# Performance work log

Measured on AMD Instinct MI355X. Metric: run time of the kernel, lower is better.

The kernel has to match this reference:

```python
import jax, jax.numpy as jnp
import numpy as np

B, T, D = 2, 2048, 1024
H = 16
HD = D // H

def setup_inputs() -> dict:
    key = jax.random.key(0)
    ks = jax.random.split(key, 6)
    s = 1.0 / np.sqrt(D)
    x  = jax.random.normal(ks[0], (B, T, D), dtype=jnp.float32)
    Wq = jax.random.uniform(ks[1], (D, D), jnp.float32, -s, s)
    Wk = jax.random.uniform(ks[2], (D, D), jnp.float32, -s, s)
    Wv = jax.random.uniform(ks[3], (D, D), jnp.float32, -s, s)
    Wo = jax.random.uniform(ks[4], (D, D), jnp.float32, -s, s)
    bo = jax.random.uniform(ks[5], (D,), jnp.float32, -s, s)
    return {"x": x, "Wq": Wq, "Wk": Wk, "Wv": Wv, "Wo": Wo, "bo": bo}

def reference(x, Wq, Wk, Wv, Wo, bo):
    b, t, d = x.shape
    # projections (no qkv bias)
    q = (x @ Wq).reshape(b, t, H, HD).transpose(0, 2, 1, 3)  # [b,h,t,hd]
    k = (x @ Wk).reshape(b, t, H, HD).transpose(0, 2, 1, 3)
    v = (x @ Wv).reshape(b, t, H, HD).transpose(0, 2, 1, 3)
    scores = jnp.einsum('bhqd,bhkd->bhqk', q, k)             # [b,h,t,t]
    causal = jnp.tril(jnp.ones((t, t), dtype=bool))
    scores = jnp.where(causal, scores, -jnp.inf)
    attn = jax.nn.softmax(scores / np.sqrt(HD), axis=-1)
    ctx = jnp.einsum('bhqk,bhkd->bhqd', attn, v)             # [b,h,t,hd]
    ctx = ctx.transpose(0, 2, 1, 3).reshape(b, t, d)
    return ctx @ Wo + bo
```

## Files before the change

kernel.cpp:

```cpp
#include <hip/hip_runtime.h>

#define Bn 2
#define Tn 2048
#define Dn 1024
#define Hn 16
#define HDn 64
#define Mn 4096

typedef __attribute__((ext_vector_type(8))) short bf16x8;
typedef __attribute__((ext_vector_type(4))) float f32x4;
typedef __attribute__((ext_vector_type(4))) unsigned int u32x4;

__device__ __forceinline__ unsigned short f2bf(float f) {
  unsigned int x = __builtin_bit_cast(unsigned int, f);
  x += 0x7FFFu + ((x >> 16) & 1u);
  return (unsigned short)(x >> 16);
}

__device__ __forceinline__ unsigned int cvtpk_bf16(float lo, float hi) {
  unsigned int r;
  asm("v_cvt_pk_bf16_f32 %0, %1, %2" : "=v"(r) : "v"(lo), "v"(hi));
  return r;
}

__device__ __forceinline__ void gload_lds16(const void* g, void* l) {
  __builtin_amdgcn_global_load_lds(
      (const __attribute__((address_space(1))) unsigned int*)g,
      (__attribute__((address_space(3))) unsigned int*)l,
      16, 0, 0);
}

__device__ __forceinline__ int rowg(int row) {
  return (((row >> 3) & 3) + 2 * (row & 3)) & 7;
}

__global__ __launch_bounds__(256) void cvt_bf16(const float* __restrict__ in,
                                                unsigned short* __restrict__ out) {
  int i = (blockIdx.x * 256 + threadIdx.x) * 4;
  float4 v = *reinterpret_cast<const float4*>(in + i);
  ushort4 o;
  o.x = f2bf(v.x); o.y = f2bf(v.y); o.z = f2bf(v.z); o.w = f2bf(v.w);
  *reinterpret_cast<ushort4*>(out + i) = o;
}

__global__ __launch_bounds__(256) void transpose4(const float* __restrict__ W0,
                                                  const float* __restrict__ W1,
                                                  const float* __restrict__ W2,
                                                  const float* __restrict__ W3,
                                                  unsigned short* __restrict__ WT) {
  __shared__ float tile[32][33];
  const int z = blockIdx.z;
  const float* W = (z == 0) ? W0 : (z == 1) ? W1 : (z == 2) ? W2 : W3;
  unsigned short* dst = WT + (size_t)z * 1048576;
  int n0 = blockIdx.x * 32, k0 = blockIdx.y * 32;
  int tx = threadIdx.x, ty = threadIdx.y;
#pragma unroll
  for (int r = ty; r < 32; r += 8)
    tile[r][tx] = W[(size_t)(k0 + r) * Dn + n0 + tx];
  __syncthreads();
#pragma unroll
  for (int r = ty; r < 32; r += 8)
    dst[(size_t)(n0 + r) * Dn + k0 + tx] = f2bf(tile[tx][r]);
}

__global__ __launch_bounds__(256) void gemm_qkv(const unsigned short* __restrict__ A,
                                                const unsigned short* __restrict__ WTall,
                                                unsigned short* __restrict__ qb,
                                                unsigned short* __restrict__ kb,
                                                unsigned short* __restrict__ vtb) {
  const int m0 = blockIdx.x * 128;
  const int n0 = blockIdx.y * 128;
  const int z  = blockIdx.z;
  const unsigned short* BT = WTall + (size_t)z * 1048576;

  __shared__ unsigned short As[128 * 32];
  __shared__ unsigned short Bs[128 * 32];

  const int tid  = threadIdx.x;
  const int lane = tid & 63;
  const int wv   = tid >> 6;
  const int wr   = wv >> 1, wc = wv & 1;
  const int l15  = lane & 15, lg = lane >> 4;

  f32x4 acc[4][4];
#pragma unroll
  for (int mi = 0; mi < 4; ++mi)
#pragma unroll
    for (int ni = 0; ni < 4; ++ni)
      acc[mi][ni] = (f32x4){0.f, 0.f, 0.f, 0.f};

  for (int kt = 0; kt < 32; ++kt) {
#pragma unroll
    for (int it = 0; it < 2; ++it) {
      int e = (it * 256 + tid) * 8;
      int r = e >> 5, c = e & 31;
      gload_lds16(A  + (size_t)(m0 + r) * Dn + kt * 32 + c,
                  (char*)As + it * 4096 + wv * 1024);
      gload_lds16(BT + (size_t)(n0 + r) * Dn + kt * 32 + c,
                  (char*)Bs + it * 4096 + wv * 1024);
    }
    __syncthreads();

    bf16x8 af[4], bf[4];
#pragma unroll
    for (int mi = 0; mi < 4; ++mi) {
      int row = wr * 64 + mi * 16 + l15;
      af[mi] = *reinterpret_cast<const bf16x8*>(&As[row * 32 + lg * 8]);
    }
#pragma unroll
    for (int ni = 0; ni < 4; ++ni) {
      int row = wc * 64 + ni * 16 + l15;
      bf[ni] = *reinterpret_cast<const bf16x8*>(&Bs[row * 32 + lg * 8]);
    }
#pragma unroll
    for (int mi = 0; mi < 4; ++mi)
#pragma unroll
      for (int ni = 0; ni < 4; ++ni)
        acc[mi][ni] = __builtin_amdgcn_mfma_f32_16x16x32_bf16(af[mi], bf[ni], acc[mi][ni], 0, 0, 0);
    __syncthreads();
  }

  unsigned short* dst = (z == 0) ? qb : (z == 1) ? kb : vtb;
#pragma unroll
  for (int mi = 0; mi < 4; ++mi)
#pragma unroll
    for (int ni = 0; ni < 4; ++ni)
#pragma unroll
      for (int j = 0; j < 4; ++j) {
        int row = m0 + wr * 64 + mi * 16 + (lg << 2) + j;
        int col = n0 + wc * 64 + ni * 16 + l15;
        int b = row >> 11, t = row & (Tn - 1);
        int h = col >> 6,  hd = col & 63;
        size_t idx = (z == 2)
          ? ((size_t)((b * Hn + h) * HDn + hd)) * Tn + t
          : ((size_t)(b * Hn + h) * Tn + t) * HDn + hd;
        dst[idx] = f2bf(acc[mi][ni][j]);
      }
}

__global__ __launch_bounds__(256) void gemm_out(const unsigned short* __restrict__ A,
                                                const unsigned short* __restrict__ BT,
                                                const float* __restrict__ bias,
                                                float* __restrict__ out) {
  const int m0 = blockIdx.x * 128;
  const int n0 = blockIdx.y * 128;

  __shared__ unsigned short As[128 * 32];
  __shared__ unsigned short Bs[128 * 32];

  const int tid  = threadIdx.x;
  const int lane = tid & 63;
  const int wv   = tid >> 6;
  const int wr   = wv >> 1, wc = wv & 1;
  const int l15  = lane & 15, lg = lane >> 4;

  f32x4 acc[4][4];
#pragma unroll
  for (int mi = 0; mi < 4; ++mi)
#pragma unroll
    for (int ni = 0; ni < 4; ++ni)
      acc[mi][ni] = (f32x4){0.f, 0.f, 0.f, 0.f};

  for (int kt = 0; kt < 32; ++kt) {
#pragma unroll
    for (int it = 0; it < 2; ++it) {
      int e = (it * 256 + tid) * 8;
      int r = e >> 5, c = e & 31;
      gload_lds16(A  + (size_t)(m0 + r) * Dn + kt * 32 + c,
                  (char*)As + it * 4096 + wv * 1024);
      gload_lds16(BT + (size_t)(n0 + r) * Dn + kt * 32 + c,
                  (char*)Bs + it * 4096 + wv * 1024);
    }
    __syncthreads();

    bf16x8 af[4], bf[4];
#pragma unroll
    for (int mi = 0; mi < 4; ++mi) {
      int row = wr * 64 + mi * 16 + l15;
      af[mi] = *reinterpret_cast<const bf16x8*>(&As[row * 32 + lg * 8]);
    }
#pragma unroll
    for (int ni = 0; ni < 4; ++ni) {
      int row = wc * 64 + ni * 16 + l15;
      bf[ni] = *reinterpret_cast<const bf16x8*>(&Bs[row * 32 + lg * 8]);
    }
#pragma unroll
    for (int mi = 0; mi < 4; ++mi)
#pragma unroll
      for (int ni = 0; ni < 4; ++ni)
        acc[mi][ni] = __builtin_amdgcn_mfma_f32_16x16x32_bf16(af[mi], bf[ni], acc[mi][ni], 0, 0, 0);
    __syncthreads();
  }

#pragma unroll
  for (int mi = 0; mi < 4; ++mi)
#pragma unroll
    for (int ni = 0; ni < 4; ++ni)
#pragma unroll
      for (int j = 0; j < 4; ++j) {
        int row = m0 + wr * 64 + mi * 16 + (lg << 2) + j;
        int col = n0 + wc * 64 + ni * 16 + l15;
        out[(size_t)row * Dn + col] = acc[mi][ni][j] + bias[col];
      }
}

__global__ __launch_bounds__(512, 4) void attn9(const unsigned short* __restrict__ q,
                                                const unsigned short* __restrict__ k,
                                                const unsigned short* __restrict__ vT,
                                                unsigned short* __restrict__ ctx) {
  __shared__ __align__(16) unsigned char smem[65536];

  const int tid  = threadIdx.x;
  const int lane = tid & 63;
  const int wv   = tid >> 6;
  const int grp  = wv >> 2;
  const int wq   = wv & 3;
  const int l15  = lane & 15, lg = lane >> 4;

  const int bid  = blockIdx.x;
  const int head = bid & 31;
  const int pr   = bid >> 5;
  const int qlo  = pr, qhi = 31 - pr;
  const int b = head >> 4, h = head & 15;

  const unsigned short* qh = q  + (size_t)head * Tn * HDn;
  const unsigned short* kh = k  + (size_t)head * Tn * HDn;
  const unsigned short* vh = vT + (size_t)head * HDn * Tn;

  const int qminL = qlo * 64 + wq * 16;
  const int qminH = qhi * 64 + wq * 16;

  bf16x8 aqL[2], aqH[2];
#pragma unroll
  for (int kc = 0; kc < 2; ++kc) {
    aqL[kc] = *reinterpret_cast<const bf16x8*>(qh + (size_t)(qminL + l15) * HDn + kc * 32 + lg * 8);
    aqH[kc] = *reinterpret_cast<const bf16x8*>(qh + (size_t)(qminH + l15) * HDn + kc * 32 + lg * 8);
  }

  f32x4 oL[4], oH[4];
#pragma unroll
  for (int n = 0; n < 4; ++n) { oL[n] = (f32x4){0.f,0.f,0.f,0.f}; oH[n] = (f32x4){0.f,0.f,0.f,0.f}; }
  float mL = -INFINITY, lL = 0.f, mH = -INFINITY, lH = 0.f;

  const float SC = 0.18033688011112042f;

  int kaddr[4][2], vaddr[4][2];
#pragma unroll
  for (int ci = 0; ci < 4; ++ci) {
    int rci = 32 * (ci >> 1) + 4 * (ci & 1) + 8 * (l15 >> 2) + (l15 & 3);
    int gk  = rowg(rci);
#pragma unroll
    for (int kc = 0; kc < 2; ++kc)
      kaddr[ci][kc] = rci * 64 + ((kc * 32 + lg * 8) ^ (gk << 3));
  }
#pragma unroll
  for (int n = 0; n < 4; ++n) {
    int rn = n * 16 + l15;
    int gv = rowg(rn);
#pragma unroll
    for (int kk = 0; kk < 2; ++kk)
      vaddr[n][kk] = rn * 64 + ((kk * 32 + lg * 8) ^ (gv << 3));
  }

  auto ksTile = [&](int buf) { return reinterpret_cast<unsigned short*>(smem + (((grp << 1) | buf) * 8192)); };
  auto vsTile = [&](int buf) { return reinterpret_cast<unsigned short*>(smem + 32768 + (((grp << 1) | buf) * 8192)); };

  auto stage = [&](int buf, int k0) {
#pragma unroll
    for (int it = 0; it < 2; ++it) {
      int o = (it * 256 + (tid & 255)) * 8;
      int row = o >> 6;
      int col = (o & 63) ^ (rowg(row) << 3);
      gload_lds16(kh + (size_t)(k0 + row) * HDn + col,
                  (char*)ksTile(buf) + (it * 2048 + wq * 512) * 2);
      gload_lds16(vh + (size_t)row * Tn + k0 + col,
                  (char*)vsTile(buf) + (it * 2048 + wq * 512) * 2);
    }
  };

  auto phase = [&](const bf16x8 (&aq)[2], int qmin, float& m, float& l,
                   f32x4 (&oacc)[4], int k0, const unsigned short* ksb,
                   const unsigned short* vsb) {
    f32x4 s[4];
#pragma unroll
    for (int ci = 0; ci < 4; ++ci) s[ci] = (f32x4){0.f, 0.f, 0.f, 0.f};
    __builtin_amdgcn_s_setprio(1);
#pragma unroll
    for (int ci = 0; ci < 4; ++ci)
#pragma unroll
      for (int kc = 0; kc < 2; ++kc) {
        bf16x8 bk = *reinterpret_cast<const bf16x8*>(&ksb[kaddr[ci][kc]]);
        s[ci] = __builtin_amdgcn_mfma_f32_16x16x32_bf16(bk, aq[kc], s[ci], 0, 0, 0);
      }
    __builtin_amdgcn_s_setprio(0);

    if (k0 + 63 > qmin) {
      const int mrel = qmin + l15 - k0 - 8 * lg;
#pragma unroll
      for (int ci = 0; ci < 4; ++ci) {
        const int koff = 32 * (ci >> 1) + 4 * (ci & 1);
#pragma unroll
        for (int r = 0; r < 4; ++r)
          if (koff + r > mrel) s[ci][r] = -INFINITY;
      }
    }
    float t0 = fmaxf(fmaxf(s[0][0], s[0][1]), fmaxf(s[0][2], s[0][3]));
    float t1 = fmaxf(fmaxf(s[1][0], s[1][1]), fmaxf(s[1][2], s[1][3]));
    float t2 = fmaxf(fmaxf(s[2][0], s[2][1]), fmaxf(s[2][2], s[2][3]));
    float t3 = fmaxf(fmaxf(s[3][0], s[3][1]), fmaxf(s[3][2], s[3][3]));
    float mraw = fmaxf(fmaxf(t0, t1), fmaxf(t2, t3));
    mraw = fmaxf(mraw, __shfl_xor(mraw, 16));
    mraw = fmaxf(mraw, __shfl_xor(mraw, 32));
    float mx = mraw * SC;
    if (!__all(mx <= m + 11.5f)) {
      float mn = fmaxf(m, mx);
      float al = exp2f(m - mn);
      l *= al;
#pragma unroll
      for (int n = 0; n < 4; ++n) oacc[n] *= al;
      m = mn;
    }
    float rs = 0.f;
    bf16x8 pb[2];
#pragma unroll
    for (int hh = 0; hh < 2; ++hh) {
      u32x4 pu;
#pragma unroll
      for (int t = 0; t < 2; ++t) {
        int ci = 2 * hh + t;
        float p0 = exp2f(__builtin_fmaf(s[ci][0], SC, -m));
        float p1 = exp2f(__builtin_fmaf(s[ci][1], SC, -m));
        float p2 = exp2f(__builtin_fmaf(s[ci][2], SC, -m));
        float p3 = exp2f(__builtin_fmaf(s[ci][3], SC, -m));
        rs += (p0 + p1) + (p2 + p3);
        pu[2 * t]     = cvtpk_bf16(p0, p1);
        pu[2 * t + 1] = cvtpk_bf16(p2, p3);
      }
      pb[hh] = __builtin_bit_cast(bf16x8, pu);
    }
    rs += __shfl_xor(rs, 16);
    rs += __shfl_xor(rs, 32);
    l += rs;

    __builtin_amdgcn_s_setprio(1);
#pragma unroll
    for (int kk = 0; kk < 2; ++kk)
#pragma unroll
      for (int n = 0; n < 4; ++n) {
        bf16x8 bv = *reinterpret_cast<const bf16x8*>(&vsb[vaddr[n][kk]]);
        oacc[n] = __builtin_amdgcn_mfma_f32_16x16x32_bf16(bv, pb[kk], oacc[n], 0, 0, 0);
      }
    __builtin_amdgcn_s_setprio(0);
  };

  const int nIt = (qhi + 2) >> 1;
  stage(0, grp << 6);
  __syncthreads();

  for (int i = 0; i < nIt; ++i) {
    const int buf = i & 1;
    const int kt  = 2 * i + grp;
    const int k0  = kt << 6;
    const int ktn = kt + 2;

    if (ktn <= qhi) stage(buf ^ 1, ktn << 6);

    if (kt <= qhi) {
      const unsigned short* ksb = ksTile(buf);
      const unsigned short* vsb = vsTile(buf);
      phase(aqH, qminH, mH, lH, oH, k0, ksb, vsb);
      if (kt <= qlo)
        phase(aqL, qminL, mL, lL, oL, k0, ksb, vsb);
    }
    __syncthreads();
  }

  float* mb = reinterpret_cast<float*>(smem);
  if (grp == 1) {
#pragma unroll
    for (int st = 0; st < 2; ++st) {
      f32x4* o = st ? oL : oH;
      int base = (((wq << 1) | st) * 64 + lane) * 19;
#pragma unroll
      for (int n = 0; n < 4; ++n)
#pragma unroll
        for (int r = 0; r < 4; ++r) mb[base + n * 4 + r] = o[n][r];
      mb[base + 16] = st ? mL : mH;
      mb[base + 17] = st ? lL : lH;
    }
  }
  __syncthreads();
  if (grp == 0) {
#pragma unroll
    for (int st = 0; st < 2; ++st) {
      f32x4* o = st ? oL : oH;
      float m0s = st ? mL : mH, l0s = st ? lL : lH;
      int qmin = st ? qminL : qminH;
      int base = (((wq << 1) | st) * 64 + lane) * 19;
      float m1s = mb[base + 16], l1s = mb[base + 17];
      float ms = fmaxf(m0s, m1s);
      float a0 = exp2f(m0s - ms), a1 = exp2f(m1s - ms);
      float li = 1.0f / (l0s * a0 + l1s * a1);
#pragma unroll
      for (int n = 0; n < 4; ++n) {
        float v0 = (o[n][0] * a0 + mb[base + n * 4 + 0] * a1) * li;
        float v1 = (o[n][1] * a0 + mb[base + n * 4 + 1] * a1) * li;
        float v2 = (o[n][2] * a0 + mb[base + n * 4 + 2] * a1) * li;
        float v3 = (o[n][3] * a0 + mb[base + n * 4 + 3] * a1) * li;
        uint2 ow = { cvtpk_bf16(v0, v1), cvtpk_bf16(v2, v3) };
        *reinterpret_cast<uint2*>(
            &ctx[(size_t)(b * Tn + qmin + l15) * Dn + h * HDn + n * 16 + 4 * lg]) = ow;
      }
    }
  }
}

extern "C" void kernel_launch(void* const* d_in, const int* in_sizes, int n_in,
                              void* d_out, int out_size, void* d_ws, size_t ws_size,
                              hipStream_t stream) {
  const float* x  = (const float*)d_in[0];
  const float* Wq = (const float*)d_in[1];
  const float* Wk = (const float*)d_in[2];
  const float* Wv = (const float*)d_in[3];
  const float* Wo = (const float*)d_in[4];
  const float* bo = (const float*)d_in[5];
  float* out = (float*)d_out;

  unsigned short* ws  = (unsigned short*)d_ws;
  unsigned short* xbf = ws;
  unsigned short* wT  = ws + 4194304;
  unsigned short* qb  = ws + 8388608;
  unsigned short* kb  = ws + 12582912;
  unsigned short* vtb = ws + 16777216;
  unsigned short* ctx = ws + 20971520;

  cvt_bf16<<<4096, 256, 0, stream>>>(x, xbf);
  transpose4<<<dim3(32, 32, 4), dim3(32, 8), 0, stream>>>(Wq, Wk, Wv, Wo, wT);

  gemm_qkv<<<dim3(32, 8, 3), 256, 0, stream>>>(xbf, wT, qb, kb, vtb);
  attn9<<<512, 512, 0, stream>>>(qb, kb, vtb, ctx);
  gemm_out<<<dim3(32, 8), 256, 0, stream>>>(ctx, wT + 3145728, bo, out);
}
```

Measured before the change: 116.6 us.

## Fuse prep kernels, use K=64 swizzled LDS tiles, and narrow the output GEMM tile

Merges the x-to-bf16 conversion and the weight transposes into one prep launch, removing a kernel launch. Both GEMMs now stage K=64 slices per iteration into XOR-swizzled LDS, which halves the number of barriers and is meant to avoid LDS bank conflicts. The output GEMM uses a 128x64 tile so it launches twice as many blocks and fills the CUs better. The cost is more LDS per block and a narrower N tile, which means less reuse of each loaded A tile in the output projection.

```diff
diff --git a/kernel.cpp b/kernel.cpp
--- a/kernel.cpp
+++ b/kernel.cpp
@@ -34,26 +34,32 @@
   return (((row >> 3) & 3) + 2 * (row & 3)) & 7;
 }
 
-__global__ __launch_bounds__(256) void cvt_bf16(const float* __restrict__ in,
-                                                unsigned short* __restrict__ out) {
-  int i = (blockIdx.x * 256 + threadIdx.x) * 4;
-  float4 v = *reinterpret_cast<const float4*>(in + i);
-  ushort4 o;
-  o.x = f2bf(v.x); o.y = f2bf(v.y); o.z = f2bf(v.z); o.w = f2bf(v.w);
-  *reinterpret_cast<ushort4*>(out + i) = o;
-}
-
-__global__ __launch_bounds__(256) void transpose4(const float* __restrict__ W0,
-                                                  const float* __restrict__ W1,
-                                                  const float* __restrict__ W2,
-                                                  const float* __restrict__ W3,
-                                                  unsigned short* __restrict__ WT) {
+__global__ __launch_bounds__(256) void prep(const float* __restrict__ x,
+                                            const float* __restrict__ W0,
+                                            const float* __restrict__ W1,
+                                            const float* __restrict__ W2,
+                                            const float* __restrict__ W3,
+                                            unsigned short* __restrict__ xbf,
+                                            unsigned short* __restrict__ WT) {
+  const int z = blockIdx.z;
+  int tx = threadIdx.x, ty = threadIdx.y;
+  if (z == 4) {
+    int tid = ty * 32 + tx;
+    size_t base = ((size_t)(blockIdx.y * 32 + blockIdx.x)) * 4096;
+#pragma unroll
+    for (int j = 0; j < 4; ++j) {
+      size_t i = base + (j * 256 + tid) * 4;
+      float4 v = *reinterpret_cast<const float4*>(x + i);
+      ushort4 o;
+      o.x = f2bf(v.x); o.y = f2bf(v.y); o.z = f2bf(v.z); o.w = f2bf(v.w);
+      *reinterpret_cast<ushort4*>(xbf + i) = o;
+    }
+    return;
+  }
   __shared__ float tile[32][33];
-  const int z = blockIdx.z;
   const float* W = (z == 0) ? W0 : (z == 1) ? W1 : (z == 2) ? W2 : W3;
   unsigned short* dst = WT + (size_t)z * 1048576;
   int n0 = blockIdx.x * 32, k0 = blockIdx.y * 32;
-  int tx = threadIdx.x, ty = threadIdx.y;
 #pragma unroll
   for (int r = ty; r < 32; r += 8)
     tile[r][tx] = W[(size_t)(k0 + r) * Dn + n0 + tx];
@@ -73,14 +79,15 @@
   const int z  = blockIdx.z;
   const unsigned short* BT = WTall + (size_t)z * 1048576;
 
-  __shared__ unsigned short As[128 * 32];
-  __shared__ unsigned short Bs[128 * 32];
+  __shared__ unsigned short As[128 * 64];
+  __shared__ unsigned short Bs[128 * 64];
 
   const int tid  = threadIdx.x;
   const int lane = tid & 63;
   const int wv   = tid >> 6;
   const int wr   = wv >> 1, wc = wv & 1;
   const int l15  = lane & 15, lg = lane >> 4;
+  const int fsw  = (l15 & 7) << 3;
 
   f32x4 acc[4][4];
 #pragma unroll
@@ -89,34 +96,36 @@
     for (int ni = 0; ni < 4; ++ni)
       acc[mi][ni] = (f32x4){0.f, 0.f, 0.f, 0.f};
 
-  for (int kt = 0; kt < 32; ++kt) {
-#pragma unroll
-    for (int it = 0; it < 2; ++it) {
+  for (int kt = 0; kt < 16; ++kt) {
+#pragma unroll
+    for (int it = 0; it < 4; ++it) {
       int e = (it * 256 + tid) * 8;
-      int r = e >> 5, c = e & 31;
-      gload_lds16(A  + (size_t)(m0 + r) * Dn + kt * 32 + c,
+      int r = e >> 6, c = e & 63;
+      int cs = c ^ ((r & 7) << 3);
+      gload_lds16(A  + (size_t)(m0 + r) * Dn + kt * 64 + cs,
                   (char*)As + it * 4096 + wv * 1024);
-      gload_lds16(BT + (size_t)(n0 + r) * Dn + kt * 32 + c,
+      gload_lds16(BT + (size_t)(n0 + r) * Dn + kt * 64 + cs,
                   (char*)Bs + it * 4096 + wv * 1024);
     }
     __syncthreads();
 
-    bf16x8 af[4], bf[4];
-#pragma unroll
-    for (int mi = 0; mi < 4; ++mi) {
-      int row = wr * 64 + mi * 16 + l15;
-      af[mi] = *reinterpret_cast<const bf16x8*>(&As[row * 32 + lg * 8]);
-    }
-#pragma unroll
-    for (int ni = 0; ni < 4; ++ni) {
-      int row = wc * 64 + ni * 16 + l15;
-      bf[ni] = *reinterpret_cast<const bf16x8*>(&Bs[row * 32 + lg * 8]);
-    }
-#pragma unroll
-    for (int mi = 0; mi < 4; ++mi)
+#pragma unroll
+    for (int kc = 0; kc < 2; ++kc) {
+      bf16x8 af[4], bf[4];
+#pragma unroll
+      for (int mi = 0; mi < 4; ++mi)
+        af[mi] = *reinterpret_cast<const bf16x8*>(
+            &As[(wr * 64 + mi * 16 + l15) * 64 + ((kc * 32 + lg * 8) ^ fsw)]);
 #pragma unroll
       for (int ni = 0; ni < 4; ++ni)
-        acc[mi][ni] = __builtin_amdgcn_mfma_f32_16x16x32_bf16(af[mi], bf[ni], acc[mi][ni], 0, 0, 0);
+        bf[ni] = *reinterpret_cast<const bf16x8*>(
+            &Bs[(wc * 64 + ni * 16 + l15) * 64 + ((kc * 32 + lg * 8) ^ fsw)]);
+#pragma unroll
+      for (int mi = 0; mi < 4; ++mi)
+#pragma unroll
+        for (int ni = 0; ni < 4; ++ni)
+          acc[mi][ni] = __builtin_amdgcn_mfma_f32_16x16x32_bf16(af[mi], bf[ni], acc[mi][ni], 0, 0, 0);
+    }
     __syncthreads();
   }
 
@@ -143,63 +152,67 @@
                                                 const float* __restrict__ bias,
                                                 float* __restrict__ out) {
   const int m0 = blockIdx.x * 128;
-  const int n0 = blockIdx.y * 128;
-
-  __shared__ unsigned short As[128 * 32];
-  __shared__ unsigned short Bs[128 * 32];
+  const int n0 = blockIdx.y * 64;
+
+  __shared__ unsigned short As[128 * 64];
+  __shared__ unsigned short Bs[64 * 64];
 
   const int tid  = threadIdx.x;
   const int lane = tid & 63;
   const int wv   = tid >> 6;
   const int wr   = wv >> 1, wc = wv & 1;
   const int l15  = lane & 15, lg = lane >> 4;
-
-  f32x4 acc[4][4];
+  const int fsw  = (l15 & 7) << 3;
+
+  f32x4 acc[4][2];
 #pragma unroll
   for (int mi = 0; mi < 4; ++mi)
 #pragma unroll
-    for (int ni = 0; ni < 4; ++ni)
+    for (int ni = 0; ni < 2; ++ni)
       acc[mi][ni] = (f32x4){0.f, 0.f, 0.f, 0.f};
 
-  for (int kt = 0; kt < 32; ++kt) {
-#pragma unroll
-    for (int it = 0; it < 2; ++it) {
+  for (int kt = 0; kt < 16; ++kt) {
+#pragma unroll
+    for (int it = 0; it < 4; ++it) {
       int e = (it * 256 + tid) * 8;
-      int r = e >> 5, c = e & 31;
-      gload_lds16(A  + (size_t)(m0 + r) * Dn + kt * 32 + c,
+      int r = e >> 6, c = e & 63;
+      int cs = c ^ ((r & 7) << 3);
+      gload_lds16(A + (size_t)(m0 + r) * Dn + kt * 64 + cs,
                   (char*)As + it * 4096 + wv * 1024);
-      gload_lds16(BT + (size_t)(n0 + r) * Dn + kt * 32 + c,
-                  (char*)Bs + it * 4096 + wv * 1024);
+      if (it < 2)
+        gload_lds16(BT + (size_t)(n0 + r) * Dn + kt * 64 + cs,
+                    (char*)Bs + it * 4096 + wv * 1024);
     }
     __syncthreads();
 
-    bf16x8 af[4], bf[4];
-#pragma unroll
-    for (int mi = 0; mi < 4; ++mi) {
-      int row = wr * 64 + mi * 16 + l15;
-      af[mi] = *reinterpret_cast<const bf16x8*>(&As[row * 32 + lg * 8]);
-    }
-#pragma unroll
-    for (int ni = 0; ni < 4; ++ni) {
-      int row = wc * 64 + ni * 16 + l15;
-      bf[ni] = *reinterpret_cast<const bf16x8*>(&Bs[row * 32 + lg * 8]);
-    }
-#pragma unroll
-    for (int mi = 0; mi < 4; ++mi)
-#pragma unroll
-      for (int ni = 0; ni < 4; ++ni)
-        acc[mi][ni] = __builtin_amdgcn_mfma_f32_16x16x32_bf16(af[mi], bf[ni], acc[mi][ni], 0, 0, 0);
+#pragma unroll
+    for (int kc = 0; kc < 2; ++kc) {
+      bf16x8 af[4], bf[2];
+#pragma unroll
+      for (int mi = 0; mi < 4; ++mi)
+        af[mi] = *reinterpret_cast<const bf16x8*>(
+            &As[(wr * 64 + mi * 16 + l15) * 64 + ((kc * 32 + lg * 8) ^ fsw)]);
+#pragma unroll
+      for (int ni = 0; ni < 2; ++ni)
+        bf[ni] = *reinterpret_cast<const bf16x8*>(
+            &Bs[(wc * 32 + ni * 16 + l15) * 64 + ((kc * 32 + lg * 8) ^ fsw)]);
+#pragma unroll
+      for (int mi = 0; mi < 4; ++mi)
+#pragma unroll
+        for (int ni = 0; ni < 2; ++ni)
+          acc[mi][ni] = __builtin_amdgcn_mfma_f32_16x16x32_bf16(af[mi], bf[ni], acc[mi][ni], 0, 0, 0);
+    }
     __syncthreads();
   }
 
 #pragma unroll
   for (int mi = 0; mi < 4; ++mi)
 #pragma unroll
-    for (int ni = 0; ni < 4; ++ni)
+    for (int ni = 0; ni < 2; ++ni)
 #pragma unroll
       for (int j = 0; j < 4; ++j) {
         int row = m0 + wr * 64 + mi * 16 + (lg << 2) + j;
-        int col = n0 + wc * 64 + ni * 16 + l15;
+        int col = n0 + wc * 32 + ni * 16 + l15;
         out[(size_t)row * Dn + col] = acc[mi][ni][j] + bias[col];
       }
 }
@@ -434,10 +447,9 @@
   unsigned short* vtb = ws + 16777216;
   unsigned short* ctx = ws + 20971520;
 
-  cvt_bf16<<<4096, 256, 0, stream>>>(x, xbf);
-  transpose4<<<dim3(32, 32, 4), dim3(32, 8), 0, stream>>>(Wq, Wk, Wv, Wo, wT);
+  prep<<<dim3(32, 32, 5), dim3(32, 8), 0, stream>>>(x, Wq, Wk, Wv, Wo, xbf, wT);
 
   gemm_qkv<<<dim3(32, 8, 3), 256, 0, stream>>>(xbf, wT, qb, kb, vtb);
   attn9<<<512, 512, 0, stream>>>(qb, kb, vtb, ctx);
-  gemm_out<<<dim3(32, 8), 256, 0, stream>>>(ctx, wT + 3145728, bo, out);
-}
+  gemm_out<<<dim3(32, 16), 256, 0, stream>>>(ctx, wT + 3145728, bo, out);
+}
```

After: 107.8 us. 1.08x faster.
